# Performance work log

Measured on AMD Instinct MI355X. Metric: run time of the kernel, lower is better.

The kernel has to match this reference:

```python
import jax, jax.numpy as jnp
import numpy as np

VOXEL_DIM = 16
CELL_DIM = 1.0
AA, A = 21, 14  # 20 amino acids + 'X'; atom14 representation
X_LBL = AA - 1  # label used for unknown residues


def make_voxel():
    v = VOXEL_DIM
    ax = jnp.arange(v, dtype=jnp.float32)
    vx = jnp.broadcast_to((ax - v / 2).reshape(-1, 1, 1), (v, v, v))
    vy = jnp.broadcast_to((ax - v / 4).reshape(1, -1, 1), (v, v, v))
    vz = jnp.broadcast_to((ax - v / 2).reshape(1, 1, -1), (v, v, v))
    return CELL_DIM * jnp.stack([vx, vy, vz], axis=3)  # (Vx,Vy,Vz,3)


def setup_inputs() -> dict:
    key = jax.random.key(0)
    k1, k2, k3, k4 = jax.random.split(key, 4)
    ZN = 1024
    C = 3.0 * jax.random.normal(k1, (ZN, A, 3), dtype=jnp.float32)
    L = jax.random.randint(k2, (ZN,), 0, AA)
    atom_mask = jnp.ones((ZN, A), dtype=jnp.float32)
    charges = 0.5 * jax.random.normal(k3, (AA, A), dtype=jnp.float32)
    return {"C": C, "L": L, "atom_mask": atom_mask, "charges": charges}


def get_backbone(C):
    n, ca, c = C[:, 0, :], C[:, 1, :], C[:, 2, :]
    b1 = ca - n
    b2 = c - ca
    b3 = jnp.cross(b1, b2)
    cb = ca - 0.58273431 * b2 + 0.56802827 * b1 - 0.54067466 * b3
    return jnp.stack([n, ca, c, cb], axis=1)  # (ZN,4,3)


def compute_frames(Cb):
    y = Cb[:, 3, :] - Cb[:, 1, :]
    y_unit = y / jnp.clip(jnp.linalg.norm(y, axis=1, keepdims=True), 1e-6)
    x_raw = Cb[:, 2, :] - Cb[:, 0, :]
    x_proj = jnp.sum(x_raw * y_unit, axis=1, keepdims=True)
    x = x_raw - x_proj
    x_unit = x / jnp.clip(jnp.linalg.norm(x, axis=1, keepdims=True), 1e-6)
    z = jnp.cross(x_unit, y_unit)
    z_unit = z / jnp.clip(jnp.linalg.norm(z, axis=1, keepdims=True), 1e-6)
    frames = jnp.stack([x_unit, y_unit, z_unit], axis=1)  # (ZN,3,3)
    return Cb[:, 3, :], frames


def compute_voxels(origins, frames, voxel):
    # rotation[n,x,y,z,s] = sum_u frames[n,u,s] * voxel[x,y,z,u]
    rot = jnp.einsum('nus,xyzu->nxyzs', frames, voxel)
    return origins[:, None, None, None, :] + rot  # (ZN,Vx,Vy,Vz,3)


def compute_fields(C, L, voxels, atom_mask, charges):
    L = jnp.where(L == -1, X_LBL, L)
    # (ZN,Vx,Vy,Vz,A,3)
    dv = voxels[:, :, :, :, None, :] - C[:, None, None, None, :, :]
    d = jnp.linalg.norm(dv, axis=-1, keepdims=True)
    dist_term = dv / (jnp.where(d == 0, 1.0, d) * jnp.clip(d, CELL_DIM) ** 2)
    pc = charges[L] * atom_mask  # (ZN,A)
    fields = jnp.einsum('na,nxyzas->nxyzs', pc, dist_term)
    fn = jnp.linalg.norm(fields, axis=-1, keepdims=True)
    fields = fields / jnp.where(fn == 0, 1.0, fn)
    return jnp.transpose(fields, (0, 4, 1, 2, 3))  # (ZN,3,Vx,Vy,Vz)


def compute_divergence(fields):
    r = CELL_DIM
    fx, fy, fz = fields[:, 0], fields[:, 1], fields[:, 2]
    dx = jnp.concatenate([
        ((fx[:, 1] - fx[:, 0]) / r)[:, None],
        (fx[:, 2:] - fx[:, :-2]) / (2 * r),
        ((fx[:, -1] - fx[:, -2]) / r)[:, None]], axis=1)
    dy = jnp.concatenate([
        ((fy[:, :, 1] - fy[:, :, 0]) / r)[:, :, None],
        (fy[:, :, 2:] - fy[:, :, :-2]) / (2 * r),
        ((fy[:, :, -1] - fy[:, :, -2]) / r)[:, :, None]], axis=2)
    dz = jnp.concatenate([
        ((fz[:, :, :, 1] - fz[:, :, :, 0]) / r)[:, :, :, None],
        (fz[:, :, :, 2:] - fz[:, :, :, :-2]) / (2 * r),
        ((fz[:, :, :, -1] - fz[:, :, :, -2]) / r)[:, :, :, None]], axis=3)
    return (dx + dy + dz)[:, None]  # (ZN,1,Vx,Vy,Vz)


def reference(C, L, atom_mask, charges):
    voxel = make_voxel()
    Cb = get_backbone(C)
    origins, frames = compute_frames(Cb)
    voxels = compute_voxels(origins, frames, voxel)
    fields = compute_fields(C, L, voxels, atom_mask, charges)
    div = compute_divergence(fields)
    return (Cb, div, frames)
```

## Files before the change

### kernel.cpp

```cpp
#include <hip/hip_runtime.h>
#include <hip/hip_bf16.h>

#define AA_NUM 21
#define A_NUM  14
#define NPTS   4096
#define BLK    256

__device__ __forceinline__ float rfl(float x) {
    return __int_as_float(__builtin_amdgcn_readfirstlane(__float_as_int(x)));
}

__global__ __launch_bounds__(BLK) void preproc_kernel(
    const float* __restrict__ Cin,
    const int*   __restrict__ Lin,
    const float* __restrict__ Min,
    const float* __restrict__ Qin,
    float*       __restrict__ out,
    int ZN)
{
    __shared__ float s_atom[A_NUM][3];
    __shared__ float s_pc[A_NUM];
    __shared__ float s_fr[12];
    __shared__ float s_fx[16][BLK];
    __shared__ float s_fy[16][BLK];

    const int n = blockIdx.x;
    const int t = threadIdx.x;
    const size_t div_off = (size_t)ZN * 12;
    const size_t fr_off  = div_off + (size_t)ZN * NPTS;

    if (t < A_NUM) {
        int la = Lin[n];
        la = (la == -1) ? (AA_NUM - 1) : la;
        s_pc[t] = Qin[la * A_NUM + t] * Min[n * A_NUM + t];
        s_atom[t][0] = Cin[(n * A_NUM + t) * 3 + 0];
        s_atom[t][1] = Cin[(n * A_NUM + t) * 3 + 1];
        s_atom[t][2] = Cin[(n * A_NUM + t) * 3 + 2];
    }
    __syncthreads();

    if (t == 0) {
        const float c0 = 0.58273431f, c1 = 0.56802827f, c2 = 0.54067466f;
        float n0x = s_atom[0][0], n0y = s_atom[0][1], n0z = s_atom[0][2];
        float cax = s_atom[1][0], cay = s_atom[1][1], caz = s_atom[1][2];
        float ccx = s_atom[2][0], ccy = s_atom[2][1], ccz = s_atom[2][2];
        float b1x = cax - n0x, b1y = cay - n0y, b1z = caz - n0z;
        float b2x = ccx - cax, b2y = ccy - cay, b2z = ccz - caz;
        float b3x = b1y * b2z - b1z * b2y;
        float b3y = b1z * b2x - b1x * b2z;
        float b3z = b1x * b2y - b1y * b2x;
        float cbx = cax - c0 * b2x + c1 * b1x - c2 * b3x;
        float cby = cay - c0 * b2y + c1 * b1y - c2 * b3y;
        float cbz = caz - c0 * b2z + c1 * b1z - c2 * b3z;

        float* po = out + (size_t)n * 12;
        po[0]  = n0x; po[1]  = n0y; po[2]  = n0z;
        po[3]  = cax; po[4]  = cay; po[5]  = caz;
        po[6]  = ccx; po[7]  = ccy; po[8]  = ccz;
        po[9]  = cbx; po[10] = cby; po[11] = cbz;

        float yx = cbx - cax, yy = cby - cay, yz = cbz - caz;
        float yr = 1.0f / fmaxf(sqrtf(yx * yx + yy * yy + yz * yz), 1e-6f);
        float yux = yx * yr, yuy = yy * yr, yuz = yz * yr;
        float xrx = ccx - n0x, xry = ccy - n0y, xrz = ccz - n0z;
        float xp = xrx * yux + xry * yuy + xrz * yuz;
        float xx = xrx - xp, xy = xry - xp, xz = xrz - xp;
        float xr = 1.0f / fmaxf(sqrtf(xx * xx + xy * xy + xz * xz), 1e-6f);
        float xux = xx * xr, xuy = xy * xr, xuz = xz * xr;
        float zx = xuy * yuz - xuz * yuy;
        float zy = xuz * yux - xux * yuz;
        float zz = xux * yuy - xuy * yux;
        float zr = 1.0f / fmaxf(sqrtf(zx * zx + zy * zy + zz * zz), 1e-6f);
        float zux = zx * zr, zuy = zy * zr, zuz = zz * zr;

        float* pf = out + fr_off + (size_t)n * 9;
        pf[0] = xux; pf[1] = xuy; pf[2] = xuz;
        pf[3] = yux; pf[4] = yuy; pf[5] = yuz;
        pf[6] = zux; pf[7] = zuy; pf[8] = zuz;

        s_fr[0] = xux; s_fr[1] = xuy; s_fr[2]  = xuz;
        s_fr[3] = yux; s_fr[4] = yuy; s_fr[5]  = yuz;
        s_fr[6] = zux; s_fr[7] = zuy; s_fr[8]  = zuz;
        s_fr[9] = cbx; s_fr[10] = cby; s_fr[11] = cbz;
    }
    __syncthreads();

    float ax[A_NUM], ay[A_NUM], az[A_NUM], aq[A_NUM];
    #pragma unroll
    for (int a = 0; a < A_NUM; ++a) {
        ax[a] = rfl(s_atom[a][0]);
        ay[a] = rfl(s_atom[a][1]);
        az[a] = rfl(s_atom[a][2]);
        aq[a] = rfl(s_pc[a]);
    }
    float fr[12];
    #pragma unroll
    for (int i = 0; i < 12; ++i) fr[i] = rfl(s_fr[i]);

    const int xi = t >> 4;
    const int yi = t & 15;
    const float vx = (float)xi - 8.0f;
    const float vy = (float)yi - 4.0f;

    float fzv[16];

    #pragma unroll
    for (int z = 0; z < 16; ++z) {
        float vz = (float)z - 8.0f;
        float px = fr[9]  + vx * fr[0] + vy * fr[3] + vz * fr[6];
        float py = fr[10] + vx * fr[1] + vy * fr[4] + vz * fr[7];
        float pz = fr[11] + vx * fr[2] + vy * fr[5] + vz * fr[8];
        float fx = 0.0f, fy = 0.0f, fz = 0.0f;
        #pragma unroll
        for (int a = 0; a < A_NUM; ++a) {
            float dx = px - ax[a], dy = py - ay[a], dz = pz - az[a];
            float d2 = dx * dx + dy * dy + dz * dz;
            float rq = __builtin_amdgcn_rsqf(d2);
            float mn = fminf(rq, 1.0f);
            float inv = rq * mn * mn;
            float w = (d2 != 0.0f) ? aq[a] * inv : 0.0f;
            fx = fmaf(w, dx, fx);
            fy = fmaf(w, dy, fy);
            fz = fmaf(w, dz, fz);
        }
        float fn2 = fx * fx + fy * fy + fz * fz;
        float rf = (fn2 != 0.0f) ? __builtin_amdgcn_rsqf(fn2) : 1.0f;
        s_fx[z][t] = fx * rf;
        s_fy[z][t] = fy * rf;
        fzv[z] = fz * rf;
    }
    __syncthreads();

    const int cxp = t + ((xi < 15) ? 16 : 0);
    const int cxm = t - ((xi > 0)  ? 16 : 0);
    const int cyp = t + ((yi < 15) ? 1  : 0);
    const int cym = t - ((yi > 0)  ? 1  : 0);
    const float sx = (xi > 0 && xi < 15) ? 0.5f : 1.0f;
    const float sy = (yi > 0 && yi < 15) ? 0.5f : 1.0f;

    float dv[16];
    #pragma unroll
    for (int z = 0; z < 16; ++z) {
        int zp = z + (z < 15), zm = z - (z > 0);
        float sz = (z > 0 && z < 15) ? 0.5f : 1.0f;
        float dxv = (s_fx[z][cxp] - s_fx[z][cxm]) * sx;
        float dyv = (s_fy[z][cyp] - s_fy[z][cym]) * sy;
        float dzv = (fzv[zp] - fzv[zm]) * sz;
        dv[z] = dxv + dyv + dzv;
    }

    float4* dout = (float4*)(out + div_off + (size_t)n * NPTS + t * 16);
    #pragma unroll
    for (int q = 0; q < 4; ++q)
        dout[q] = make_float4(dv[4 * q], dv[4 * q + 1], dv[4 * q + 2], dv[4 * q + 3]);
}

extern "C" void kernel_launch(void* const* d_in, const int* in_sizes, int n_in,
                              void* d_out, int out_size, void* d_ws, size_t ws_size,
                              hipStream_t stream) {
    const float* C = (const float*)d_in[0];
    const int*   L = (const int*)d_in[1];
    const float* M = (const float*)d_in[2];
    const float* Q = (const float*)d_in[3];
    float* out = (float*)d_out;
    const int ZN = in_sizes[1];
    preproc_kernel<<<dim3(ZN), dim3(BLK), 0, stream>>>(C, L, M, Q, out, ZN);
}
```

Before: 101.9 us.

## Split each residue's voxel grid into two z-halves across blocks with halo

Launches two blocks per residue, each computing 8 z-slices plus one halo slice of the field, so there are twice as many blocks and each thread carries less per-thread state. The z-component now goes through shared memory instead of registers so the halo can be used for the z-derivative. The cost is recomputing one extra z-slice per block (9 of 8) and repeating the frame setup in both blocks. The per-block z loop is no longer unrolled.

```diff
diff --git a/kernel.cpp b/kernel.cpp
--- a/kernel.cpp
+++ b/kernel.cpp
@@ -1,5 +1,4 @@
 #include <hip/hip_runtime.h>
-#include <hip/hip_bf16.h>
 
 #define AA_NUM 21
 #define A_NUM  14
@@ -21,10 +20,15 @@
     __shared__ float s_atom[A_NUM][3];
     __shared__ float s_pc[A_NUM];
     __shared__ float s_fr[12];
-    __shared__ float s_fx[16][BLK];
-    __shared__ float s_fy[16][BLK];
+    __shared__ float s_fx[8][BLK];
+    __shared__ float s_fy[8][BLK];
+    __shared__ float s_fz[9][BLK];
 
-    const int n = blockIdx.x;
+    const int n    = blockIdx.x >> 1;
+    const int half = blockIdx.x & 1;
+    const int zlo  = half << 3;
+    const int zmin = half ? 7 : 0;
+    const int off  = half;
     const int t = threadIdx.x;
     const size_t div_off = (size_t)ZN * 12;
     const size_t fr_off  = div_off + (size_t)ZN * NPTS;
@@ -53,12 +57,6 @@
         float cby = cay - c0 * b2y + c1 * b1y - c2 * b3y;
         float cbz = caz - c0 * b2z + c1 * b1z - c2 * b3z;
 
-        float* po = out + (size_t)n * 12;
-        po[0]  = n0x; po[1]  = n0y; po[2]  = n0z;
-        po[3]  = cax; po[4]  = cay; po[5]  = caz;
-        po[6]  = ccx; po[7]  = ccy; po[8]  = ccz;
-        po[9]  = cbx; po[10] = cby; po[11] = cbz;
-
         float yx = cbx - cax, yy = cby - cay, yz = cbz - caz;
         float yr = 1.0f / fmaxf(sqrtf(yx * yx + yy * yy + yz * yz), 1e-6f);
         float yux = yx * yr, yuy = yy * yr, yuz = yz * yr;
@@ -73,10 +71,17 @@
         float zr = 1.0f / fmaxf(sqrtf(zx * zx + zy * zy + zz * zz), 1e-6f);
         float zux = zx * zr, zuy = zy * zr, zuz = zz * zr;
 
-        float* pf = out + fr_off + (size_t)n * 9;
-        pf[0] = xux; pf[1] = xuy; pf[2] = xuz;
-        pf[3] = yux; pf[4] = yuy; pf[5] = yuz;
-        pf[6] = zux; pf[7] = zuy; pf[8] = zuz;
+        if (half == 0) {
+            float* po = out + (size_t)n * 12;
+            po[0]  = n0x; po[1]  = n0y; po[2]  = n0z;
+            po[3]  = cax; po[4]  = cay; po[5]  = caz;
+            po[6]  = ccx; po[7]  = ccy; po[8]  = ccz;
+            po[9]  = cbx; po[10] = cby; po[11] = cbz;
+            float* pf = out + fr_off + (size_t)n * 9;
+            pf[0] = xux; pf[1] = xuy; pf[2] = xuz;
+            pf[3] = yux; pf[4] = yuy; pf[5] = yuz;
+            pf[6] = zux; pf[7] = zuy; pf[8] = zuz;
+        }
 
         s_fr[0] = xux; s_fr[1] = xuy; s_fr[2]  = xuz;
         s_fr[3] = yux; s_fr[4] = yuy; s_fr[5]  = yuz;
@@ -101,15 +106,15 @@
     const int yi = t & 15;
     const float vx = (float)xi - 8.0f;
     const float vy = (float)yi - 4.0f;
+    const float bpx = fr[9]  + vx * fr[0] + vy * fr[3];
+    const float bpy = fr[10] + vx * fr[1] + vy * fr[4];
+    const float bpz = fr[11] + vx * fr[2] + vy * fr[5];
 
-    float fzv[16];
-
-    #pragma unroll
-    for (int z = 0; z < 16; ++z) {
-        float vz = (float)z - 8.0f;
-        float px = fr[9]  + vx * fr[0] + vy * fr[3] + vz * fr[6];
-        float py = fr[10] + vx * fr[1] + vy * fr[4] + vz * fr[7];
-        float pz = fr[11] + vx * fr[2] + vy * fr[5] + vz * fr[8];
+    for (int l = 0; l < 9; ++l) {
+        float vz = (float)(zmin + l) - 8.0f;
+        float px = fmaf(vz, fr[6], bpx);
+        float py = fmaf(vz, fr[7], bpy);
+        float pz = fmaf(vz, fr[8], bpz);
         float fx = 0.0f, fy = 0.0f, fz = 0.0f;
         #pragma unroll
         for (int a = 0; a < A_NUM; ++a) {
@@ -125,9 +130,12 @@
         }
         float fn2 = fx * fx + fy * fy + fz * fz;
         float rf = (fn2 != 0.0f) ? __builtin_amdgcn_rsqf(fn2) : 1.0f;
-        s_fx[z][t] = fx * rf;
-        s_fy[z][t] = fy * rf;
-        fzv[z] = fz * rf;
+        s_fz[l][t] = fz * rf;
+        int li = l - off;
+        if (li >= 0 && li < 8) {
+            s_fx[li][t] = fx * rf;
+            s_fy[li][t] = fy * rf;
+        }
     }
     __syncthreads();
 
@@ -138,21 +146,23 @@
     const float sx = (xi > 0 && xi < 15) ? 0.5f : 1.0f;
     const float sy = (yi > 0 && yi < 15) ? 0.5f : 1.0f;
 
-    float dv[16];
+    float dv[8];
     #pragma unroll
-    for (int z = 0; z < 16; ++z) {
-        int zp = z + (z < 15), zm = z - (z > 0);
+    for (int i = 0; i < 8; ++i) {
+        int z = zlo + i;
+        int l = i + off;
+        int lzp = l + (z < 15);
+        int lzm = l - (z > 0);
         float sz = (z > 0 && z < 15) ? 0.5f : 1.0f;
-        float dxv = (s_fx[z][cxp] - s_fx[z][cxm]) * sx;
-        float dyv = (s_fy[z][cyp] - s_fy[z][cym]) * sy;
-        float dzv = (fzv[zp] - fzv[zm]) * sz;
-        dv[z] = dxv + dyv + dzv;
+        float dxv = (s_fx[i][cxp] - s_fx[i][cxm]) * sx;
+        float dyv = (s_fy[i][cyp] - s_fy[i][cym]) * sy;
+        float dzv = (s_fz[lzp][t] - s_fz[lzm][t]) * sz;
+        dv[i] = dxv + dyv + dzv;
     }
 
-    float4* dout = (float4*)(out + div_off + (size_t)n * NPTS + t * 16);
-    #pragma unroll
-    for (int q = 0; q < 4; ++q)
-        dout[q] = make_float4(dv[4 * q], dv[4 * q + 1], dv[4 * q + 2], dv[4 * q + 3]);
+    float4* dout = (float4*)(out + div_off + (size_t)n * NPTS + t * 16 + zlo);
+    dout[0] = make_float4(dv[0], dv[1], dv[2], dv[3]);
+    dout[1] = make_float4(dv[4], dv[5], dv[6], dv[7]);
 }
 
 extern "C" void kernel_launch(void* const* d_in, const int* in_sizes, int n_in,
@@ -164,5 +174,5 @@
     const float* Q = (const float*)d_in[3];
     float* out = (float*)d_out;
     const int ZN = in_sizes[1];
-    preproc_kernel<<<dim3(ZN), dim3(BLK), 0, stream>>>(C, L, M, Q, out, ZN);
+    preproc_kernel<<<dim3(2 * ZN), dim3(BLK), 0, stream>>>(C, L, M, Q, out, ZN);
 }
```

New measurement: 97.34 us. 1.05x faster.

## Split z-columns across thread pairs and compute frames redundantly per thread

Applied to the files above, without the earlier changes.

Doubles the block to 512 threads so each pair of threads handles one (x,y) column, with each thread computing 8 of the 16 z points. The z-derivative halo is exchanged with a lane shuffle. The backbone and frame setup is now computed redundantly by every thread from global loads, which removes two shared-memory round trips and their barriers. This raises parallelism and lowers per-thread register pressure, at the cost of redundant setup arithmetic and more global load instructions.

```diff
diff --git a/kernel.cpp b/kernel.cpp
--- a/kernel.cpp
+++ b/kernel.cpp
@@ -1,16 +1,15 @@
 #include <hip/hip_runtime.h>
-#include <hip/hip_bf16.h>
 
 #define AA_NUM 21
 #define A_NUM  14
 #define NPTS   4096
-#define BLK    256
+#define BLK    512
 
 __device__ __forceinline__ float rfl(float x) {
     return __int_as_float(__builtin_amdgcn_readfirstlane(__float_as_int(x)));
 }
 
-__global__ __launch_bounds__(BLK) void preproc_kernel(
+__global__ __launch_bounds__(BLK, 8) void preproc_kernel(
     const float* __restrict__ Cin,
     const int*   __restrict__ Lin,
     const float* __restrict__ Min,
@@ -18,98 +17,91 @@
     float*       __restrict__ out,
     int ZN)
 {
-    __shared__ float s_atom[A_NUM][3];
-    __shared__ float s_pc[A_NUM];
-    __shared__ float s_fr[12];
-    __shared__ float s_fx[16][BLK];
-    __shared__ float s_fy[16][BLK];
+    __shared__ float s_fx[16][256];
+    __shared__ float s_fy[16][256];
 
     const int n = blockIdx.x;
     const int t = threadIdx.x;
+    const int col = t >> 1;
+    const int h   = t & 1;
+    const int xi  = col >> 4;
+    const int yi  = col & 15;
     const size_t div_off = (size_t)ZN * 12;
     const size_t fr_off  = div_off + (size_t)ZN * NPTS;
 
-    if (t < A_NUM) {
-        int la = Lin[n];
-        la = (la == -1) ? (AA_NUM - 1) : la;
-        s_pc[t] = Qin[la * A_NUM + t] * Min[n * A_NUM + t];
-        s_atom[t][0] = Cin[(n * A_NUM + t) * 3 + 0];
-        s_atom[t][1] = Cin[(n * A_NUM + t) * 3 + 1];
-        s_atom[t][2] = Cin[(n * A_NUM + t) * 3 + 2];
-    }
-    __syncthreads();
+    const float* c = Cin + (size_t)n * A_NUM * 3;
+    int la = Lin[n];
+    la = (la == -1) ? (AA_NUM - 1) : la;
+    const float* qrow = Qin + la * A_NUM;
+    const float* mrow = Min + (size_t)n * A_NUM;
+
+    const float c0 = 0.58273431f, c1 = 0.56802827f, c2 = 0.54067466f;
+    float n0x = c[0], n0y = c[1], n0z = c[2];
+    float cax = c[3], cay = c[4], caz = c[5];
+    float ccx = c[6], ccy = c[7], ccz = c[8];
+    float b1x = cax - n0x, b1y = cay - n0y, b1z = caz - n0z;
+    float b2x = ccx - cax, b2y = ccy - cay, b2z = ccz - caz;
+    float b3x = b1y * b2z - b1z * b2y;
+    float b3y = b1z * b2x - b1x * b2z;
+    float b3z = b1x * b2y - b1y * b2x;
+    float cbx = cax - c0 * b2x + c1 * b1x - c2 * b3x;
+    float cby = cay - c0 * b2y + c1 * b1y - c2 * b3y;
+    float cbz = caz - c0 * b2z + c1 * b1z - c2 * b3z;
+
+    float yx = cbx - cax, yy = cby - cay, yz = cbz - caz;
+    float yr = 1.0f / fmaxf(sqrtf(yx * yx + yy * yy + yz * yz), 1e-6f);
+    float yux = yx * yr, yuy = yy * yr, yuz = yz * yr;
+    float xrx = ccx - n0x, xry = ccy - n0y, xrz = ccz - n0z;
+    float xp = xrx * yux + xry * yuy + xrz * yuz;
+    float xx = xrx - xp, xy = xry - xp, xz = xrz - xp;
+    float xr = 1.0f / fmaxf(sqrtf(xx * xx + xy * xy + xz * xz), 1e-6f);
+    float xux = xx * xr, xuy = xy * xr, xuz = xz * xr;
+    float zx = xuy * yuz - xuz * yuy;
+    float zy = xuz * yux - xux * yuz;
+    float zz = xux * yuy - xuy * yux;
+    float zr = 1.0f / fmaxf(sqrtf(zx * zx + zy * zy + zz * zz), 1e-6f);
+    float zux = zx * zr, zuy = zy * zr, zuz = zz * zr;
 
     if (t == 0) {
-        const float c0 = 0.58273431f, c1 = 0.56802827f, c2 = 0.54067466f;
-        float n0x = s_atom[0][0], n0y = s_atom[0][1], n0z = s_atom[0][2];
-        float cax = s_atom[1][0], cay = s_atom[1][1], caz = s_atom[1][2];
-        float ccx = s_atom[2][0], ccy = s_atom[2][1], ccz = s_atom[2][2];
-        float b1x = cax - n0x, b1y = cay - n0y, b1z = caz - n0z;
-        float b2x = ccx - cax, b2y = ccy - cay, b2z = ccz - caz;
-        float b3x = b1y * b2z - b1z * b2y;
-        float b3y = b1z * b2x - b1x * b2z;
-        float b3z = b1x * b2y - b1y * b2x;
-        float cbx = cax - c0 * b2x + c1 * b1x - c2 * b3x;
-        float cby = cay - c0 * b2y + c1 * b1y - c2 * b3y;
-        float cbz = caz - c0 * b2z + c1 * b1z - c2 * b3z;
-
         float* po = out + (size_t)n * 12;
         po[0]  = n0x; po[1]  = n0y; po[2]  = n0z;
         po[3]  = cax; po[4]  = cay; po[5]  = caz;
         po[6]  = ccx; po[7]  = ccy; po[8]  = ccz;
         po[9]  = cbx; po[10] = cby; po[11] = cbz;
-
-        float yx = cbx - cax, yy = cby - cay, yz = cbz - caz;
-        float yr = 1.0f / fmaxf(sqrtf(yx * yx + yy * yy + yz * yz), 1e-6f);
-        float yux = yx * yr, yuy = yy * yr, yuz = yz * yr;
-        float xrx = ccx - n0x, xry = ccy - n0y, xrz = ccz - n0z;
-        float xp = xrx * yux + xry * yuy + xrz * yuz;
-        float xx = xrx - xp, xy = xry - xp, xz = xrz - xp;
-        float xr = 1.0f / fmaxf(sqrtf(xx * xx + xy * xy + xz * xz), 1e-6f);
-        float xux = xx * xr, xuy = xy * xr, xuz = xz * xr;
-        float zx = xuy * yuz - xuz * yuy;
-        float zy = xuz * yux - xux * yuz;
-        float zz = xux * yuy - xuy * yux;
-        float zr = 1.0f / fmaxf(sqrtf(zx * zx + zy * zy + zz * zz), 1e-6f);
-        float zux = zx * zr, zuy = zy * zr, zuz = zz * zr;
-
         float* pf = out + fr_off + (size_t)n * 9;
         pf[0] = xux; pf[1] = xuy; pf[2] = xuz;
         pf[3] = yux; pf[4] = yuy; pf[5] = yuz;
         pf[6] = zux; pf[7] = zuy; pf[8] = zuz;
+    }
 
-        s_fr[0] = xux; s_fr[1] = xuy; s_fr[2]  = xuz;
-        s_fr[3] = yux; s_fr[4] = yuy; s_fr[5]  = yuz;
-        s_fr[6] = zux; s_fr[7] = zuy; s_fr[8]  = zuz;
-        s_fr[9] = cbx; s_fr[10] = cby; s_fr[11] = cbz;
-    }
-    __syncthreads();
+    float fr0 = rfl(xux), fr1 = rfl(xuy), fr2 = rfl(xuz);
+    float fr3 = rfl(yux), fr4 = rfl(yuy), fr5 = rfl(yuz);
+    float fr6 = rfl(zux), fr7 = rfl(zuy), fr8 = rfl(zuz);
+    float orx = rfl(cbx), ory = rfl(cby), orz = rfl(cbz);
 
     float ax[A_NUM], ay[A_NUM], az[A_NUM], aq[A_NUM];
     #pragma unroll
     for (int a = 0; a < A_NUM; ++a) {
-        ax[a] = rfl(s_atom[a][0]);
-        ay[a] = rfl(s_atom[a][1]);
-        az[a] = rfl(s_atom[a][2]);
-        aq[a] = rfl(s_pc[a]);
+        ax[a] = c[a * 3 + 0];
+        ay[a] = c[a * 3 + 1];
+        az[a] = c[a * 3 + 2];
+        aq[a] = rfl(qrow[a] * mrow[a]);
     }
-    float fr[12];
-    #pragma unroll
-    for (int i = 0; i < 12; ++i) fr[i] = rfl(s_fr[i]);
 
-    const int xi = t >> 4;
-    const int yi = t & 15;
     const float vx = (float)xi - 8.0f;
     const float vy = (float)yi - 4.0f;
+    const float bpx = orx + vx * fr0 + vy * fr3;
+    const float bpy = ory + vx * fr1 + vy * fr4;
+    const float bpz = orz + vx * fr2 + vy * fr5;
 
-    float fzv[16];
+    float fzv[8];
+    const int zbase = h << 3;
 
-    #pragma unroll
-    for (int z = 0; z < 16; ++z) {
-        float vz = (float)z - 8.0f;
-        float px = fr[9]  + vx * fr[0] + vy * fr[3] + vz * fr[6];
-        float py = fr[10] + vx * fr[1] + vy * fr[4] + vz * fr[7];
-        float pz = fr[11] + vx * fr[2] + vy * fr[5] + vz * fr[8];
+    for (int i = 0; i < 8; ++i) {
+        float vz = (float)(zbase + i) - 8.0f;
+        float px = fmaf(vz, fr6, bpx);
+        float py = fmaf(vz, fr7, bpy);
+        float pz = fmaf(vz, fr8, bpz);
         float fx = 0.0f, fy = 0.0f, fz = 0.0f;
         #pragma unroll
         for (int a = 0; a < A_NUM; ++a) {
@@ -125,34 +117,38 @@
         }
         float fn2 = fx * fx + fy * fy + fz * fz;
         float rf = (fn2 != 0.0f) ? __builtin_amdgcn_rsqf(fn2) : 1.0f;
-        s_fx[z][t] = fx * rf;
-        s_fy[z][t] = fy * rf;
-        fzv[z] = fz * rf;
+        s_fx[zbase + i][col] = fx * rf;
+        s_fy[zbase + i][col] = fy * rf;
+        fzv[i] = fz * rf;
     }
+
+    float halo = __shfl_xor(h ? fzv[0] : fzv[7], 1);
+
     __syncthreads();
 
-    const int cxp = t + ((xi < 15) ? 16 : 0);
-    const int cxm = t - ((xi > 0)  ? 16 : 0);
-    const int cyp = t + ((yi < 15) ? 1  : 0);
-    const int cym = t - ((yi > 0)  ? 1  : 0);
+    const int cxp = col + ((xi < 15) ? 16 : 0);
+    const int cxm = col - ((xi > 0)  ? 16 : 0);
+    const int cyp = col + ((yi < 15) ? 1  : 0);
+    const int cym = col - ((yi > 0)  ? 1  : 0);
     const float sx = (xi > 0 && xi < 15) ? 0.5f : 1.0f;
     const float sy = (yi > 0 && yi < 15) ? 0.5f : 1.0f;
 
-    float dv[16];
+    float dv[8];
     #pragma unroll
-    for (int z = 0; z < 16; ++z) {
-        int zp = z + (z < 15), zm = z - (z > 0);
+    for (int i = 0; i < 8; ++i) {
+        int z = zbase + i;
+        float up = (i < 7) ? fzv[i + 1] : (h ? fzv[7] : halo);
+        float dn = (i > 0) ? fzv[i - 1] : (h ? halo : fzv[0]);
         float sz = (z > 0 && z < 15) ? 0.5f : 1.0f;
+        float dzv = (up - dn) * sz;
         float dxv = (s_fx[z][cxp] - s_fx[z][cxm]) * sx;
         float dyv = (s_fy[z][cyp] - s_fy[z][cym]) * sy;
-        float dzv = (fzv[zp] - fzv[zm]) * sz;
-        dv[z] = dxv + dyv + dzv;
+        dv[i] = dxv + dyv + dzv;
     }
 
-    float4* dout = (float4*)(out + div_off + (size_t)n * NPTS + t * 16);
-    #pragma unroll
-    for (int q = 0; q < 4; ++q)
-        dout[q] = make_float4(dv[4 * q], dv[4 * q + 1], dv[4 * q + 2], dv[4 * q + 3]);
+    float4* dout = (float4*)(out + div_off + (size_t)n * NPTS + col * 16 + (h << 3));
+    dout[0] = make_float4(dv[0], dv[1], dv[2], dv[3]);
+    dout[1] = make_float4(dv[4], dv[5], dv[6], dv[7]);
 }
 
 extern "C" void kernel_launch(void* const* d_in, const int* in_sizes, int n_in,
```

Measured after the change: 98.95 us. 2.9% less time.
